# Kernel optimization log

Hardware: AMD Instinct MI355X
Metric: run time of the kernel (lower is better)

## Reference

```python
import jax, jax.numpy as jnp
import numpy as np

N = 65536   # number of input points
M = 4096    # subsample_size (centroids)
K = 64      # group_limit (neighborhood size)
RADIUS = 0.2  # group_radius


def _mlp(x, W1, b1, W2, b2, W3, b3):
    # PyG MLP([6, 64, 64, 128], act='relu'); batch_norm with default running
    # stats (mean 0, var 1) is identity, so: Linear-ReLU-Linear-ReLU-Linear.
    h = jax.nn.relu(x @ W1 + b1)
    h = jax.nn.relu(h @ W2 + b2)
    return h @ W3 + b3


def setup_inputs() -> dict:
    key = jax.random.key(0)
    ks = jax.random.split(key, 8)
    vertices = jax.random.normal(ks[0], (N, 3), dtype=jnp.float32)
    centroid_indices = jax.random.randint(ks[1], (M,), 0, N)

    def lin(k, fi, fo):
        return (jax.random.normal(k, (fi, fo), dtype=jnp.float32) / np.sqrt(fi)).astype(jnp.float32)

    return {
        "vertices": vertices,
        "centroid_indices": centroid_indices,
        "W1": lin(ks[2], 6, 64),  "b1": jnp.zeros((64,), jnp.float32),
        "W2": lin(ks[3], 64, 64), "b2": jnp.zeros((64,), jnp.float32),
        "W3": lin(ks[4], 64, 128), "b3": jnp.zeros((128,), jnp.float32),
    }


def reference(vertices, centroid_indices, W1, b1, W2, b2, W3, b3):
    # --- group_around_centroids ---
    sq_norm = jnp.einsum('ij,ij->i', vertices, vertices)          # [N]
    cpos = vertices[centroid_indices]                              # [M,3]
    # faithful distance formula: sqrt(|sn_c - 2 c.v + sn|)
    d = jnp.sqrt(jnp.abs(sq_norm[centroid_indices][:, None]
                         - 2.0 * (cpos @ vertices.T)
                         + sq_norm[None, :]))                      # [M,N]  (~1 GB)
    # K nearest per centroid (equivalent to masking by k-th sorted distance)
    neg_dk, idx = jax.lax.top_k(-d, K)                             # [M,K]
    d_k = -neg_dk                                                  # ascending distances
    limit = jnp.minimum(d_k[:, K - 1], RADIUS)                     # [M]
    mask = d_k <= limit[:, None]                                   # [M,K]

    # --- PointNetConv: msg = MLP(cat[x_j, pos_j - pos_i]), max-aggregate to centroid ---
    pos_j = vertices[idx]                                          # [M,K,3]
    feat = jnp.concatenate([pos_j, pos_j - cpos[:, None, :]], axis=-1)  # [M,K,6]
    h = _mlp(feat, W1, b1, W2, b2, W3, b3)                         # [M,K,128]
    h = jnp.where(mask[:, :, None], h, -jnp.inf)
    return jnp.max(h, axis=1)                                      # [M,128]
```

## Files before the change

kernel.cpp:

```cpp
#include <hip/hip_runtime.h>
#include <hip/hip_bf16.h>

#define GD     50
#define NC     (GD*GD*GD)
#define CHUNK  250
#define CAPK   256
#define RADIUS_F 0.2f
#define R2SAFE 0.0401f

typedef unsigned long long ull;
typedef __attribute__((ext_vector_type(4))) _Float16 f16x4;
typedef __attribute__((ext_vector_type(8))) _Float16 f16x8;
typedef __attribute__((ext_vector_type(4))) float    f32x4;

__device__ __forceinline__ int cellcoord(float v) {
    int c = (int)floorf((v + 5.0f) * 5.0f);
    return min(max(c, 0), GD - 1);
}


__global__ void sa_zero_kernel(int4* __restrict__ dst, int n4) {
    int i = blockIdx.x * blockDim.x + threadIdx.x;
    int stride = gridDim.x * blockDim.x;
    for (; i < n4; i += stride) dst[i] = make_int4(0, 0, 0, 0);
}

__global__ void sa_prep_kernel(const float* __restrict__ vtx,
                               float4* __restrict__ pt4,
                               int* __restrict__ cid,
                               int* __restrict__ cellCnt,
                               int N,
                               const float* __restrict__ W1,
                               const float* __restrict__ W2,
                               const float* __restrict__ W3,
                               _Float16* __restrict__ wf16) {
    int i = blockIdx.x * blockDim.x + threadIdx.x;
    int stride = gridDim.x * blockDim.x;
    for (int p = i; p < N; p += stride) {
        float x = vtx[3 * p], y = vtx[3 * p + 1], z = vtx[3 * p + 2];
        float sn = fmaf(z, z, fmaf(y, y, x * x));
        pt4[p] = make_float4(x, y, z, sn);
        int cc = (cellcoord(z) * GD + cellcoord(y)) * GD + cellcoord(x);
        cid[p] = cc;
        atomicAdd(&cellCnt[cc], 1);
    }
    for (int e = i; e < 1024; e += stride) {
        int nn = e >> 8, lane = (e >> 2) & 63, j = e & 3;
        int col = nn * 16 + (lane & 15), k = (lane >> 4) * 4 + j;
        wf16[e] = (k < 6) ? (_Float16)W1[k * 64 + col] : (_Float16)0.f;
    }
    for (int e = i; e < 2048; e += stride) {
        int nn = e >> 9, lane = (e >> 3) & 63, j = e & 7;
        int col = nn * 16 + (lane & 15), k = (lane >> 4) * 8 + j;
        wf16[1024 + e] = (_Float16)W2[k * 64 + col];
        wf16[3072 + e] = (_Float16)W2[(k + 32) * 64 + col];
    }
    for (int e = i; e < 4096; e += stride) {
        int nn = e >> 9, lane = (e >> 3) & 63, j = e & 7;
        int col = nn * 16 + (lane & 15), k = (lane >> 4) * 8 + j;
        wf16[5120 + e] = (_Float16)W3[k * 128 + col];
        wf16[9216 + e] = (_Float16)W3[(k + 32) * 128 + col];
    }
}

__global__ __launch_bounds__(256) void sa_offsets_kernel(
    const int* __restrict__ cellCnt, int* __restrict__ cellStart,
    int* __restrict__ cellEnd, int* __restrict__ cellCur,
    int* __restrict__ cursor) {
    __shared__ int sc[256];
    __shared__ int base_s;
    int t = threadIdx.x;
    int i = blockIdx.x * CHUNK + t;
    int c = (t < CHUNK) ? cellCnt[i] : 0;
    sc[t] = c;
    __syncthreads();
    for (int d = 1; d < 256; d <<= 1) {
        int o = (t >= d) ? sc[t - d] : 0;
        __syncthreads();
        sc[t] += o;
        __syncthreads();
    }
    if (t == 255) base_s = atomicAdd(cursor, sc[255]);
    __syncthreads();
    int start = base_s + sc[t] - c;
    if (t < CHUNK) {
        cellStart[i] = start;
        cellEnd[i] = start + c;
        cellCur[i] = start;
    }
}

__global__ void sa_scatter_kernel(const float4* __restrict__ pt4,
                                  const int* __restrict__ cid,
                                  int* __restrict__ cellCur,
                                  float4* __restrict__ sorted4,
                                  int* __restrict__ sidx,
                                  const int* __restrict__ cidx,
                                  float4* __restrict__ cpos4,
                                  int N, int M) {
    int p = blockIdx.x * blockDim.x + threadIdx.x;
    if (p < N) {
        int pos = atomicAdd(&cellCur[cid[p]], 1);
        sorted4[pos] = pt4[p];
        sidx[pos] = p;
    }
    if (p < M) cpos4[p] = pt4[cidx[p]];
}

__global__ __launch_bounds__(64) void sa_fused2_kernel(
    const float4* __restrict__ pt4, const float4* __restrict__ cpos4,
    const float4* __restrict__ sorted4, const int* __restrict__ sidx,
    const int* __restrict__ cellStart, const int* __restrict__ cellEnd,
    const _Float16* __restrict__ wf16,
    const float* __restrict__ b1, const float* __restrict__ b2,
    const float* __restrict__ b3, float* __restrict__ out) {

    __shared__ __align__(16) char smem[8192];
    __shared__ int selb[64];
    __shared__ int chdesc[64];
    __shared__ int scnt_s;

    int lane = threadIdx.x;
    int c = blockIdx.x;
    float4 cc = cpos4[c];

    ull* key = (ull*)smem;
    _Float16* featb = (_Float16*)(smem + 4096);
    _Float16* h = (_Float16*)smem;

    int cx = cellcoord(cc.x), cy = cellcoord(cc.y), cz = cellcoord(cc.z);
    int x0 = max(cx - 1, 0), x1 = min(cx + 1, GD - 1), lx = x1 - x0 + 1;
    int y0 = max(cy - 1, 0), y1 = min(cy + 1, GD - 1), ly = y1 - y0 + 1;
    int z0 = max(cz - 1, 0), z1 = min(cz + 1, GD - 1), lz = z1 - z0 + 1;
    int nrow = ly * lz;

    int rstart = 0, rlen = 0;
    if (lane < nrow) {
        int iy = lane % ly, iz = lane / ly;
        int gy = y0 + iy, gz = z0 + iz;
        float ylo = (gy == 0) ? -1e30f : gy * 0.2f - 5.0f;
        float yhi = (gy == GD - 1) ? 1e30f : (gy + 1) * 0.2f - 5.0f;
        float zlo = (gz == 0) ? -1e30f : gz * 0.2f - 5.0f;
        float zhi = (gz == GD - 1) ? 1e30f : (gz + 1) * 0.2f - 5.0f;
        float dy = fmaxf(0.f, fmaxf(ylo - cc.y, cc.y - yhi));
        float dz = fmaxf(0.f, fmaxf(zlo - cc.z, cc.z - zhi));
        if (fmaf(dz, dz, dy * dy) <= R2SAFE) {
            int cell0 = (gz * GD + gy) * GD + x0;
            int cellL = cell0 + (lx - 1);
            rstart = cellStart[cell0];
            rlen = cellEnd[cellL] - rstart;
        }
    }
    if (lane == 0) scnt_s = 0;

    int nch = (rlen + 63) >> 6;
    int ip = nch;
#pragma unroll
    for (int d = 1; d < 16; d <<= 1) {
        int o = __shfl_up(ip, d);
        if (lane >= d) ip += o;
    }
    int C = __shfl(ip, nrow - 1);
    int ebase = ip - nch;
    if (lane < nrow) {
        for (int k = 0; k < nch; ++k) {
            int st = rstart + (k << 6);
            int ln = min(64, rlen - (k << 6));
            chdesc[ebase + k] = st | (ln << 20);
        }
    }

#pragma unroll 2
    for (int ch = 0; ch < C; ++ch) {
        int d0 = chdesc[ch];
        int st = d0 & 0xFFFFF, ln = d0 >> 20;
        if (lane < ln) {
            int sp = st + lane;
            float4 p = sorted4[sp];
            int pid = sidx[sp];
            float dot = fmaf(p.z, cc.z, fmaf(p.y, cc.y, p.x * cc.x));
            float tt = fmaf(-2.f, dot, cc.w) + p.w;
            if (tt <= R2SAFE) {
                float dd = sqrtf(fabsf(tt));
                if (dd <= RADIUS_F) {
                    int slot = atomicAdd(&scnt_s, 1);
                    if (slot < CAPK)
                        key[slot] = (((ull)__float_as_uint(dd)) << 32) | (unsigned)pid;
                }
            }
        }
    }

    int n = min(scnt_s, CAPK);
    int nsel = min(n, 64);
    if (n > 64) {
        for (int i = lane; i < n; i += 64) {
            ull ki = key[i];
            int r = 0;
            for (int j = 0; j < n; ++j) r += (key[j] < ki) ? 1 : 0;
            if (r < 64) selb[r] = (int)(unsigned)(ki & 0xffffffffu);
        }
    } else {
        for (int i = lane; i < n; i += 64)
            selb[i] = (int)(unsigned)(key[i] & 0xffffffffu);
    }

    {
        _Float16 z = (_Float16)0.f;
        f16x8 lo8 = {z, z, z, z, z, z, z, z};
        if (lane < nsel) {
            float4 p = pt4[selb[lane]];
            lo8[0] = (_Float16)p.x; lo8[1] = (_Float16)p.y; lo8[2] = (_Float16)p.z;
            lo8[3] = (_Float16)(p.x - cc.x);
            lo8[4] = (_Float16)(p.y - cc.y);
            lo8[5] = (_Float16)(p.z - cc.z);
        }
        f16x8 hi8 = {z, z, z, z, z, z, z, z};
        *(f16x8*)&featb[lane * 16 + 0] = lo8;
        *(f16x8*)&featb[lane * 16 + 8] = hi8;
    }

    int r16 = lane & 15, g = lane >> 4;

    {
        f16x4 a1[4];
#pragma unroll
        for (int m = 0; m < 4; ++m)
            a1[m] = *(const f16x4*)&featb[(m * 16 + r16) * 16 + g * 4];
#pragma unroll
        for (int nn = 0; nn < 4; ++nn) {
            int col = nn * 16 + r16;
            f16x4 b = *(const f16x4*)&wf16[(nn * 64 + lane) * 4];
            float bb = b1[col];
#pragma unroll
            for (int m = 0; m < 4; ++m) {
                f32x4 acc = {bb, bb, bb, bb};
                acc = __builtin_amdgcn_mfma_f32_16x16x16f16(a1[m], b, acc, 0, 0, 0);
#pragma unroll
                for (int reg = 0; reg < 4; ++reg) {
                    int row = m * 16 + g * 4 + reg;
                    h[row * 64 + (col ^ ((row & 7) << 3))] =
                        (_Float16)fmaxf(acc[reg], 0.f);
                }
            }
        }
    }

    {
        f16x8 a2[4][2];
#pragma unroll
        for (int m = 0; m < 4; ++m)
#pragma unroll
            for (int kt = 0; kt < 2; ++kt) {
                int row = m * 16 + r16;
                int k0 = kt * 32 + g * 8;
                a2[m][kt] = *(const f16x8*)&h[row * 64 + (k0 ^ ((row & 7) << 3))];
            }
#pragma unroll
        for (int nn = 0; nn < 4; ++nn) {
            int col = nn * 16 + r16;
            f16x8 bA = *(const f16x8*)&wf16[1024 + (nn * 64 + lane) * 8];
            f16x8 bB = *(const f16x8*)&wf16[3072 + (nn * 64 + lane) * 8];
            float bb = b2[col];
#pragma unroll
            for (int m = 0; m < 4; ++m) {
                f32x4 acc = {bb, bb, bb, bb};
                acc = __builtin_amdgcn_mfma_f32_16x16x32_f16(a2[m][0], bA, acc, 0, 0, 0);
                acc = __builtin_amdgcn_mfma_f32_16x16x32_f16(a2[m][1], bB, acc, 0, 0, 0);
#pragma unroll
                for (int reg = 0; reg < 4; ++reg) {
                    int row = m * 16 + g * 4 + reg;
                    h[row * 64 + (col ^ ((row & 7) << 3))] =
                        (_Float16)fmaxf(acc[reg], 0.f);
                }
            }
        }
    }

    {
        f16x8 a3[4][2];
#pragma unroll
        for (int m = 0; m < 4; ++m)
#pragma unroll
            for (int kt = 0; kt < 2; ++kt) {
                int row = m * 16 + r16;
                int k0 = kt * 32 + g * 8;
                a3[m][kt] = *(const f16x8*)&h[row * 64 + (k0 ^ ((row & 7) << 3))];
            }
        float ninf = __int_as_float(0xff800000);
#pragma unroll
        for (int nn = 0; nn < 8; ++nn) {
            int col = nn * 16 + r16;
            f16x8 bA = *(const f16x8*)&wf16[5120 + (nn * 64 + lane) * 8];
            f16x8 bB = *(const f16x8*)&wf16[9216 + (nn * 64 + lane) * 8];
            float bb = b3[col];
            float vm = ninf;
#pragma unroll
            for (int m = 0; m < 4; ++m) {
                f32x4 acc = {bb, bb, bb, bb};
                acc = __builtin_amdgcn_mfma_f32_16x16x32_f16(a3[m][0], bA, acc, 0, 0, 0);
                acc = __builtin_amdgcn_mfma_f32_16x16x32_f16(a3[m][1], bB, acc, 0, 0, 0);
#pragma unroll
                for (int reg = 0; reg < 4; ++reg) {
                    int row = m * 16 + g * 4 + reg;
                    if (row < nsel) vm = fmaxf(vm, acc[reg]);
                }
            }
            vm = fmaxf(vm, __shfl_xor(vm, 16));
            vm = fmaxf(vm, __shfl_xor(vm, 32));
            if (lane < 16) out[(size_t)c * 128 + nn * 16 + lane] = vm;
        }
    }
}

extern "C" void kernel_launch(void* const* d_in, const int* in_sizes, int n_in,
                              void* d_out, int out_size, void* d_ws, size_t ws_size,
                              hipStream_t stream) {
    const float* vtx = (const float*)d_in[0];
    const int* cidx  = (const int*)d_in[1];
    const float* W1  = (const float*)d_in[2];
    const float* b1  = (const float*)d_in[3];
    const float* W2  = (const float*)d_in[4];
    const float* b2  = (const float*)d_in[5];
    const float* W3  = (const float*)d_in[6];
    const float* b3  = (const float*)d_in[7];
    float* out = (float*)d_out;

    int N = in_sizes[0] / 3;
    int M = in_sizes[1];

    char* ws = (char*)d_ws;
    size_t off = 0;
    float4* pt4     = (float4*)(ws + off); off += (size_t)N * 16;
    float4* sorted4 = (float4*)(ws + off); off += (size_t)N * 16;
    float4* cpos4   = (float4*)(ws + off); off += (size_t)M * 16;
    int* sidx       = (int*)(ws + off);    off += (size_t)N * 4;
    int* cid        = (int*)(ws + off);    off += (size_t)N * 4;
    int* cellCnt    = (int*)(ws + off);    off += (size_t)NC * 4;
    int* cursor     = (int*)(ws + off);    off += 16;
    int* cellStart  = (int*)(ws + off);    off += (size_t)NC * 4;
    int* cellEnd    = (int*)(ws + off);    off += (size_t)NC * 4;
    int* cellCur    = (int*)(ws + off);    off += (size_t)NC * 4;
    _Float16* wf16  = (_Float16*)(ws + off);

    sa_zero_kernel<<<256, 256, 0, stream>>>((int4*)cellCnt, (NC * 4 + 16) / 16);
    sa_prep_kernel<<<512, 256, 0, stream>>>(vtx, pt4, cid, cellCnt, N,
                                            W1, W2, W3, wf16);
    sa_offsets_kernel<<<NC / CHUNK, 256, 0, stream>>>(cellCnt, cellStart,
                                                      cellEnd, cellCur, cursor);
    sa_scatter_kernel<<<(N + 255) / 256, 256, 0, stream>>>(pt4, cid, cellCur,
                                                           sorted4, sidx,
                                                           cidx, cpos4, N, M);
    sa_fused2_kernel<<<M, 64, 0, stream>>>(pt4, cpos4, sorted4, sidx,
                                           cellStart, cellEnd, wf16,
                                           b1, b2, b3, out);
}
```

Baseline: 75.69 us.

## Split neighbor collection from MLP and stage weights in shared memory

Splits the fused per-centroid kernel into two: a collection kernel that finds and ranks the neighbors and writes selected indices to global memory, and an MLP kernel that processes four centroids per 256-thread block. The MLP kernel loads the fp16 weights and biases into shared memory once per block, so each wave no longer fetches them from global memory. The rank-selection loop is padded to a multiple of 64 with sentinel keys and unrolled by 8. The cost is an extra launch, a global round trip for the selection indices, and larger shared-memory use that may lower occupancy.

```diff
diff --git a/kernel.cpp b/kernel.cpp
--- a/kernel.cpp
+++ b/kernel.cpp
@@ -107,15 +107,13 @@
     if (p < M) cpos4[p] = pt4[cidx[p]];
 }
 
-__global__ __launch_bounds__(64) void sa_fused2_kernel(
-    const float4* __restrict__ pt4, const float4* __restrict__ cpos4,
+__global__ __launch_bounds__(64) void sa_collect_kernel(
+    const float4* __restrict__ cpos4,
     const float4* __restrict__ sorted4, const int* __restrict__ sidx,
     const int* __restrict__ cellStart, const int* __restrict__ cellEnd,
-    const _Float16* __restrict__ wf16,
-    const float* __restrict__ b1, const float* __restrict__ b2,
-    const float* __restrict__ b3, float* __restrict__ out) {
-
-    __shared__ __align__(16) char smem[8192];
+    int* __restrict__ selG, int* __restrict__ nselG) {
+
+    __shared__ __align__(16) ull key[CAPK + 64];
     __shared__ int selb[64];
     __shared__ int chdesc[64];
     __shared__ int scnt_s;
@@ -123,10 +121,6 @@
     int lane = threadIdx.x;
     int c = blockIdx.x;
     float4 cc = cpos4[c];
-
-    ull* key = (ull*)smem;
-    _Float16* featb = (_Float16*)(smem + 4096);
-    _Float16* h = (_Float16*)smem;
 
     int cx = cellcoord(cc.x), cy = cellcoord(cc.y), cz = cellcoord(cc.z);
     int x0 = max(cx - 1, 0), x1 = min(cx + 1, GD - 1), lx = x1 - x0 + 1;
@@ -193,11 +187,17 @@
 
     int n = min(scnt_s, CAPK);
     int nsel = min(n, 64);
+    int n64 = (n + 63) & ~63;
+    if (lane < n64 - n) key[n + lane] = ~0ull;
     if (n > 64) {
         for (int i = lane; i < n; i += 64) {
             ull ki = key[i];
             int r = 0;
-            for (int j = 0; j < n; ++j) r += (key[j] < ki) ? 1 : 0;
+            for (int j = 0; j < n64; j += 8) {
+#pragma unroll
+                for (int jj = 0; jj < 8; ++jj)
+                    r += (key[j + jj] < ki) ? 1 : 0;
+            }
             if (r < 64) selb[r] = (int)(unsigned)(ki & 0xffffffffu);
         }
     } else {
@@ -205,33 +205,64 @@
             selb[i] = (int)(unsigned)(key[i] & 0xffffffffu);
     }
 
+    if (lane < nsel) selG[(size_t)c * 64 + lane] = selb[lane];
+    if (lane == 0) nselG[c] = nsel;
+}
+
+__global__ __launch_bounds__(256) void sa_mlp3_kernel(
+    const float4* __restrict__ pt4, const float4* __restrict__ cpos4,
+    const int* __restrict__ selG, const int* __restrict__ nselG,
+    const _Float16* __restrict__ wf16,
+    const float* __restrict__ b1, const float* __restrict__ b2,
+    const float* __restrict__ b3, float* __restrict__ out) {
+
+    __shared__ __align__(16) _Float16 Wf[13312];
+    __shared__ __align__(16) float    Wb[256];
+    __shared__ __align__(16) _Float16 featb[4][1024];
+    __shared__ __align__(16) _Float16 hb[4][4096];
+
+    int t = threadIdx.x, w = t >> 6, lane = t & 63;
+    int r16 = lane & 15, g = lane >> 4;
+    int c = blockIdx.x * 4 + w;
+
+    {
+        const uint4* src = (const uint4*)wf16;
+        uint4* dst = (uint4*)Wf;
+        for (int i = t; i < 13312 / 8; i += 256) dst[i] = src[i];
+        if (t < 64) Wb[t] = b1[t];
+        else if (t < 128) Wb[t] = b2[t - 64];
+        else Wb[t] = b3[t - 128];
+    }
+    int nsel = nselG[c];
+    float4 cc = cpos4[c];
     {
         _Float16 z = (_Float16)0.f;
         f16x8 lo8 = {z, z, z, z, z, z, z, z};
         if (lane < nsel) {
-            float4 p = pt4[selb[lane]];
+            float4 p = pt4[selG[(size_t)c * 64 + lane]];
             lo8[0] = (_Float16)p.x; lo8[1] = (_Float16)p.y; lo8[2] = (_Float16)p.z;
             lo8[3] = (_Float16)(p.x - cc.x);
             lo8[4] = (_Float16)(p.y - cc.y);
             lo8[5] = (_Float16)(p.z - cc.z);
         }
         f16x8 hi8 = {z, z, z, z, z, z, z, z};
-        *(f16x8*)&featb[lane * 16 + 0] = lo8;
-        *(f16x8*)&featb[lane * 16 + 8] = hi8;
-    }
-
-    int r16 = lane & 15, g = lane >> 4;
+        *(f16x8*)&featb[w][lane * 16 + 0] = lo8;
+        *(f16x8*)&featb[w][lane * 16 + 8] = hi8;
+    }
+    __syncthreads();
+
+    _Float16* h = hb[w];
 
     {
         f16x4 a1[4];
 #pragma unroll
         for (int m = 0; m < 4; ++m)
-            a1[m] = *(const f16x4*)&featb[(m * 16 + r16) * 16 + g * 4];
+            a1[m] = *(const f16x4*)&featb[w][(m * 16 + r16) * 16 + g * 4];
 #pragma unroll
         for (int nn = 0; nn < 4; ++nn) {
             int col = nn * 16 + r16;
-            f16x4 b = *(const f16x4*)&wf16[(nn * 64 + lane) * 4];
-            float bb = b1[col];
+            f16x4 b = *(const f16x4*)&Wf[(nn * 64 + lane) * 4];
+            float bb = Wb[col];
 #pragma unroll
             for (int m = 0; m < 4; ++m) {
                 f32x4 acc = {bb, bb, bb, bb};
@@ -259,9 +290,9 @@
 #pragma unroll
         for (int nn = 0; nn < 4; ++nn) {
             int col = nn * 16 + r16;
-            f16x8 bA = *(const f16x8*)&wf16[1024 + (nn * 64 + lane) * 8];
-            f16x8 bB = *(const f16x8*)&wf16[3072 + (nn * 64 + lane) * 8];
-            float bb = b2[col];
+            f16x8 bA = *(const f16x8*)&Wf[1024 + (nn * 64 + lane) * 8];
+            f16x8 bB = *(const f16x8*)&Wf[3072 + (nn * 64 + lane) * 8];
+            float bb = Wb[64 + col];
 #pragma unroll
             for (int m = 0; m < 4; ++m) {
                 f32x4 acc = {bb, bb, bb, bb};
@@ -291,9 +322,9 @@
 #pragma unroll
         for (int nn = 0; nn < 8; ++nn) {
             int col = nn * 16 + r16;
-            f16x8 bA = *(const f16x8*)&wf16[5120 + (nn * 64 + lane) * 8];
-            f16x8 bB = *(const f16x8*)&wf16[9216 + (nn * 64 + lane) * 8];
-            float bb = b3[col];
+            f16x8 bA = *(const f16x8*)&Wf[5120 + (nn * 64 + lane) * 8];
+            f16x8 bB = *(const f16x8*)&Wf[9216 + (nn * 64 + lane) * 8];
+            float bb = Wb[128 + col];
             float vm = ninf;
 #pragma unroll
             for (int m = 0; m < 4; ++m) {
@@ -341,6 +372,8 @@
     int* cellStart  = (int*)(ws + off);    off += (size_t)NC * 4;
     int* cellEnd    = (int*)(ws + off);    off += (size_t)NC * 4;
     int* cellCur    = (int*)(ws + off);    off += (size_t)NC * 4;
+    int* selG       = (int*)(ws + off);    off += (size_t)M * 64 * 4;
+    int* nselG      = (int*)(ws + off);    off += (size_t)M * 4;
     _Float16* wf16  = (_Float16*)(ws + off);
 
     sa_zero_kernel<<<256, 256, 0, stream>>>((int4*)cellCnt, (NC * 4 + 16) / 16);
@@ -351,7 +384,8 @@
     sa_scatter_kernel<<<(N + 255) / 256, 256, 0, stream>>>(pt4, cid, cellCur,
                                                            sorted4, sidx,
                                                            cidx, cpos4, N, M);
-    sa_fused2_kernel<<<M, 64, 0, stream>>>(pt4, cpos4, sorted4, sidx,
-                                           cellStart, cellEnd, wf16,
-                                           b1, b2, b3, out);
-}
+    sa_collect_kernel<<<M, 64, 0, stream>>>(cpos4, sorted4, sidx,
+                                            cellStart, cellEnd, selG, nselG);
+    sa_mlp3_kernel<<<M / 4, 256, 0, stream>>>(pt4, cpos4, selG, nselG, wf16,
+                                              b1, b2, b3, out);
+}
```

New measurement: 71.81 us. -5.1%, faster.
